# Kernel tuning notes

Hardware: AMD Instinct MI355X
Metric: run time of the kernel (lower is better)

## Reference

```python
import math
import jax, jax.numpy as jnp
import numpy as np

B_IN, B_OUT = 16, 16
F_IN, F_OUT, BATCH = 32, 64, 4
N_ALPHA, N_GAMMA = 4, 3
KERNEL_BETA = math.pi / 8.0
L_TOT = sum((2 * l + 1) ** 2 for l in range(B_OUT))  # 5456


def _lg(n):
    return math.lgamma(n + 1.0)


def _small_d(l, beta):
    """Wigner small-d matrix d^l_{m,n}(beta), [2l+1, 2l+1], Condon-Shortley phase."""
    c, s = math.cos(0.5 * beta), math.sin(0.5 * beta)
    d = np.zeros((2 * l + 1, 2 * l + 1), dtype=np.float64)
    for mi, m in enumerate(range(-l, l + 1)):
        for ni, n in enumerate(range(-l, l + 1)):
            pref = 0.5 * (_lg(l + m) + _lg(l - m) + _lg(l + n) + _lg(l - n))
            acc = 0.0
            for k in range(max(0, n - m), min(l + n, l - m) + 1):
                ln = pref - _lg(l + n - k) - _lg(k) - _lg(m - n + k) - _lg(l - m - k)
                acc += ((-1.0) ** (m - n + k)) * math.exp(ln) * (c ** (2 * l + n - m - 2 * k)) * (s ** (m - n + 2 * k))
            d[mi, ni] = acc
    return d


def _qweights(b):
    """Kostelec-Rockmore SOFT quadrature weights over the 2b beta samples."""
    k = np.arange(b)
    w = np.array([
        (2.0 / b) * math.sin(math.pi * (2 * j + 1) / (4.0 * b)) *
        np.sum(np.sin((2 * j + 1) * (2 * k + 1) * math.pi / (4.0 * b)) / (2 * k + 1))
        for j in range(2 * b)])
    return w


def _wigner_table(betas, b_out, scale_fn):
    rows = []
    for beta in betas:
        blocks = [(_small_d(l, beta) * scale_fn(l)).ravel() for l in range(b_out)]
        rows.append(np.concatenate(blocks))
    return np.stack(rows)  # [len(betas), L_TOT]


def _grid_basis(grid, b_out):
    """conj(D^l_{mn}(a,b,g)) = e^{+i m a} d^l_{mn}(b) e^{+i n g}, flattened over (l,m,n)."""
    cols = []
    for (a, bb, g) in grid:
        blocks = []
        for l in range(b_out):
            m = np.arange(-l, l + 1)
            d = _small_d(l, bb)
            ph = np.exp(1j * (m[:, None] * a + m[None, :] * g))
            blocks.append((d * ph).ravel())
        cols.append(np.concatenate(blocks))
    return np.stack(cols, axis=1)  # [L_TOT, n_grid] complex


def _freq_indices(b_out, nfft):
    ms, ns = [], []
    for l in range(b_out):
        r = np.arange(-l, l + 1)
        M, N = np.meshgrid(r, r, indexing='ij')
        ms.append(np.mod(M.ravel(), nfft))
        ns.append(np.mod(N.ravel(), nfft))
    return np.concatenate(ms), np.concatenate(ns)


def make_grid():
    alphas = [2.0 * math.pi * i / N_ALPHA for i in range(N_ALPHA)]
    gammas = [2.0 * math.pi * i / N_GAMMA for i in range(N_GAMMA)]
    return [(a, KERNEL_BETA, g) for a in alphas for g in gammas]


def setup_inputs() -> dict:
    key = jax.random.key(0)
    k1, k2 = jax.random.split(key)
    x = jax.random.normal(k1, (BATCH, F_IN, 2 * B_IN, 2 * B_IN, 2 * B_IN), jnp.float32)
    grid = make_grid()
    n_grid = len(grid)
    stdv = 1.0 / math.sqrt(n_grid * F_IN * (B_OUT ** 3) / float(B_IN ** 3))
    kernel = stdv * jax.random.normal(k2, (F_IN, F_OUT, n_grid), jnp.float32)
    bias = jnp.zeros((1, F_OUT, 1, 1, 1), jnp.float32)
    # analysis table: quadrature weight * d, with (2pi/2b)^2/(8pi^2) = 1/(8 b^2) absorbed
    betas_in = np.pi * (2 * np.arange(2 * B_IN) + 1) / (4.0 * B_IN)
    w = _qweights(B_IN) / (8.0 * B_IN ** 2)
    wig_f = _wigner_table(betas_in, B_OUT, lambda l: 1.0) * w[:, None]
    # synthesis table: (2l+1) * d, times (2b)^2 to cancel ifft2 normalization
    betas_out = np.pi * (2 * np.arange(2 * B_OUT) + 1) / (4.0 * B_OUT)
    wig_i = _wigner_table(betas_out, B_OUT, lambda l: (2 * l + 1) * (2 * B_OUT) ** 2)
    D = _grid_basis(grid, B_OUT)
    return {
        'x': x, 'kernel': kernel, 'bias': bias,
        'wigner_fwd': jnp.asarray(wig_f, jnp.float32),
        'wigner_inv': jnp.asarray(wig_i, jnp.float32),
        'D_re': jnp.asarray(D.real, jnp.float32),
        'D_im': jnp.asarray(D.imag, jnp.float32),
    }


def reference(x, kernel, bias, wigner_fwd, wigner_inv, D_re, D_im):
    batch, fin = x.shape[0], x.shape[1]
    fout = kernel.shape[1]
    midx_in, nidx_in = _freq_indices(B_OUT, 2 * B_IN)
    midx_out, nidx_out = _freq_indices(B_OUT, 2 * B_OUT)
    # --- SO3 FFT of input: FFT over (alpha, gamma), weighted beta-sum with Wigner-d ---
    Xf = jnp.fft.fft2(x.astype(jnp.complex64), axes=(-2, -1))   # [z,i,beta,ma,ng]
    Xg = Xf[..., midx_in, nidx_in]                               # [z,i,beta,L]
    xh = jnp.einsum('bl,zibl->lzi', wigner_fwd.astype(jnp.complex64), Xg)  # [L,z,i]
    # --- local FT of kernel on SO(3) grid points ---
    Dc = jax.lax.complex(D_re, D_im)                             # [L, n_grid]
    yh = jnp.einsum('lj,ioj->lio', Dc, kernel.astype(jnp.complex64))       # [L,i,o]
    # --- per-frequency block matmul (SO3_mm): z^l = x^l @ y^l, contracting f_in ---
    zs, begin = [], 0
    for l in range(B_OUT):
        n = 2 * l + 1
        xl = xh[begin:begin + n * n].reshape(n, n, batch, fin)
        yl = yh[begin:begin + n * n].reshape(n, n, fin, fout)
        zs.append(jnp.einsum('mkzi,knio->mnzo', xl, yl).reshape(n * n, batch, fout))
        begin += n * n
    zh = jnp.concatenate(zs, axis=0)                             # [L,z,o]
    # --- inverse SO3 FFT: scatter (l,m,n) -> FFT bins, ifft over (alpha,gamma) ---
    term = jnp.einsum('bl,lzo->zobl', wigner_inv.astype(jnp.complex64), zh)
    ng = 2 * B_OUT
    Zf = jnp.zeros((batch, fout, ng, ng, ng), jnp.complex64)
    Zf = Zf.at[..., midx_out, nidx_out].add(term)
    out = jnp.fft.ifft2(Zf, axes=(-2, -1)).real.astype(x.dtype)
    return out + bias
```

## Files before the change

### kernel.cpp

```cpp
#include <hip/hip_runtime.h>
#include <math.h>


typedef unsigned short u16;
typedef unsigned int   u32;
typedef __attribute__((ext_vector_type(8))) short  short8;
typedef __attribute__((ext_vector_type(4))) float  floatx4;
typedef __attribute__((ext_vector_type(2))) float  f32x2;

constexpr int LTOT = 5456;

constexpr int LB[17] = {0,1,10,35,84,165,286,455,680,969,
                        1330,1771,2300,2925,3654,4495,5456};

__device__ inline u16 f2bf(float f) {
    u32 u = __float_as_uint(f);
    u += 0x7fff + ((u >> 16) & 1);
    return (u16)(u >> 16);
}
__device__ inline u32 pack2bf(float re, float im) {
    return (u32)f2bf(re) | ((u32)f2bf(im) << 16);
}

__device__ inline short8 btr4(uint4 q, u32 sel, u32 msk) {
    uint4 t;
    t.x = __builtin_amdgcn_perm(q.x, q.x, sel) ^ msk;
    t.y = __builtin_amdgcn_perm(q.y, q.y, sel) ^ msk;
    t.z = __builtin_amdgcn_perm(q.z, q.z, sel) ^ msk;
    t.w = __builtin_amdgcn_perm(q.w, q.w, sel) ^ msk;
    return *(short8*)&t;
}

__device__ __forceinline__ f32x2 cfma(f32x2 e, f32x2 t, f32x2 acc) {
    asm("v_pk_fma_f32 %0, %1, %2, %0 op_sel:[0,0,0] op_sel_hi:[0,1,1]\n\t"
        "v_pk_fma_f32 %0, %1, %2, %0 op_sel:[1,1,0] op_sel_hi:[1,0,1] neg_lo:[0,1,0]"
        : "+v"(acc) : "v"(e), "v"(t));
    return acc;
}
__device__ __forceinline__ f32x2 cmulp(f32x2 t, f32x2 r) {
    f32x2 d;
    asm("v_pk_mul_f32 %0, %1, %2 op_sel:[0,0] op_sel_hi:[0,1]\n\t"
        "v_pk_fma_f32 %0, %1, %2, %0 op_sel:[1,1,0] op_sel_hi:[1,0,1] neg_lo:[0,1,0]"
        : "=&v"(d) : "v"(t), "v"(r));
    return d;
}
__device__ __forceinline__ f32x2 fma_bl(f32x2 w2, f32x2 v, f32x2 acc) {
    asm("v_pk_fma_f32 %0, %1, %2, %0 op_sel:[0,0,0] op_sel_hi:[0,1,1]"
        : "+v"(acc) : "v"(w2), "v"(v));
    return acc;
}
__device__ __forceinline__ f32x2 fma_bh(f32x2 w2, f32x2 v, f32x2 acc) {
    asm("v_pk_fma_f32 %0, %1, %2, %0 op_sel:[1,0,0] op_sel_hi:[1,1,1]"
        : "+v"(acc) : "v"(w2), "v"(v));
    return acc;
}

__global__ __launch_bounds__(256) void k_wtr(const float* __restrict__ w,
                                             float* __restrict__ wT) {
    int t  = blockIdx.x * 256 + threadIdx.x;
    int bq = blockIdx.y;
    if (t < LTOT) {
        float4 v;
        v.x = w[(size_t)(bq * 4 + 0) * LTOT + t];
        v.y = w[(size_t)(bq * 4 + 1) * LTOT + t];
        v.z = w[(size_t)(bq * 4 + 2) * LTOT + t];
        v.w = w[(size_t)(bq * 4 + 3) * LTOT + t];
        *(float4*)(wT + ((size_t)bq * LTOT + t) * 4) = v;
    }
}

__global__ __launch_bounds__(512) void k_fft_fwd(const float* __restrict__ x,
                                                 u32* __restrict__ Xfb) {
    __shared__ __align__(8) float xs[1088];
    __shared__ __align__(8) f32x2 Gc[1056];
    __shared__ f32x2 Wfc[32];
    int tid = threadIdx.x;
    if (tid < 32) {
        float sv, cv;
        sincosf(6.28318530717958647692f * (float)tid / 32.0f, &sv, &cv);
        f32x2 wv; wv.x = cv; wv.y = -sv;
        Wfc[tid] = wv;
    }
    const float* src = x + (size_t)blockIdx.x * 1024;
    for (int e = tid; e < 1024; e += 512) xs[(e >> 5) * 34 + (e & 31)] = src[e];
    __syncthreads();
    {
        int a = tid >> 4, k = tid & 15;
        const f32x2* rowp = (const f32x2*)&xs[a * 34];
        f32x2 r = Wfc[2 * k];
        f32x2 p0 = rowp[0];
        f32x2 E; E.x = p0.x; E.y = 0.f;
        f32x2 O; O.x = p0.y; O.y = 0.f;
        f32x2 t = r;
#pragma unroll
        for (int h = 1; h < 16; h++) {
            f32x2 p = rowp[h];
            E = fma_bl(p, t, E);
            O = fma_bh(p, t, O);
            if (h < 15) t = cmulp(t, r);
        }
        f32x2 WO = cmulp(O, Wfc[k]);
        Gc[a * 33 + k]      = E + WO;
        Gc[a * 33 + k + 16] = E - WO;
    }
    __syncthreads();
    {
        u32* dst = Xfb + (size_t)blockIdx.x * 512;
        int ng = tid & 31, ma = tid >> 5;
        f32x2 r = Wfc[2 * ma];
        f32x2 E = Gc[ng];
        f32x2 O = Gc[33 + ng];
        f32x2 t = r;
#pragma unroll
        for (int h = 1; h < 16; h++) {
            f32x2 e = Gc[(2 * h) * 33 + ng];
            f32x2 o = Gc[(2 * h + 1) * 33 + ng];
            E = cfma(e, t, E);
            O = cfma(o, t, O);
            if (h < 15) t = cmulp(t, r);
        }
        f32x2 WO = cmulp(O, Wfc[ma]);
        dst[ma * 32 + ng] = pack2bf(E.x + WO.x, E.y + WO.y);
    }
}

__global__ __launch_bounds__(256) void k_prep_B(const float* __restrict__ Dre,
                                                const float* __restrict__ Dim,
                                                const float* __restrict__ ker,
                                                u32* __restrict__ yhb) {
    __shared__ float Ds[2][24];
    int t0  = blockIdx.x * 2;
    int tid = threadIdx.x;
    if (tid < 48) {
        int rr = tid / 24, jj = tid - rr * 24;
        Ds[rr][jj] = (jj < 12) ? Dre[(t0 + rr) * 12 + jj] : Dim[(t0 + rr) * 12 + jj - 12];
    }
    __syncthreads();
    for (int rep = 0; rep < 8; rep++) {
        int io = rep * 256 + tid;
        int i  = io >> 6, o = io & 63;
        int nio = ((i >> 4) << 10) + ((o >> 5) << 9) + (((o >> 3) & 3) << 7)
                + (((i >> 2) & 3) << 5) + ((o & 7) << 2) + (i & 3);
        const float4* kp = (const float4*)(ker + io * 12);
        float4 ka = kp[0], kb = kp[1], kc = kp[2];
        float kv[12] = {ka.x, ka.y, ka.z, ka.w, kb.x, kb.y, kb.z, kb.w,
                        kc.x, kc.y, kc.z, kc.w};
#pragma unroll
        for (int rr = 0; rr < 2; rr++) {
            float sr = 0.f, si = 0.f;
#pragma unroll
            for (int j = 0; j < 12; j++) {
                sr += Ds[rr][j]      * kv[j];
                si += Ds[rr][12 + j] * kv[j];
            }
            yhb[(size_t)(t0 + rr) * 2048 + nio] = pack2bf(sr, si);
        }
    }
}

__global__ __launch_bounds__(256) void k_beta_A(const u32* __restrict__ Xfb,
                                                const float* __restrict__ wfT,
                                                u16* __restrict__ Ab) {
    int ma  = blockIdx.x >> 6;
    int zig = blockIdx.x & 63;
    int tid = threadIdx.x;
    int ng  = tid & 31;
    int lq  = (tid >> 5) & 3;
    int zil = tid >> 7;
    int zi  = zig * 2 + zil;
    int z = zi >> 5, i = zi & 31;
    int mh = (ma <= 15) ? ma : ma - 32;
    int nh = (ng <= 15) ? ng : ng - 32;
    int am = mh < 0 ? -mh : mh;
    int an = nh < 0 ? -nh : nh;
    int l0 = am > an ? am : an;
    int lb = lq * 4;

    int isconj = (ma > 16);
    int mau = isconj ? (32 - ma) : ma;
    int ngu = isconj ? ((32 - ng) & 31) : ng;
    if (mau > 15) { mau = 0; ngu = 0; }

    int tl[4];
#pragma unroll
    for (int j = 0; j < 4; j++) {
        int l = lb + j;
        tl[j] = LB[l] + (mh + l) * (2 * l + 1) + (nh + l);
    }
    float2 acc[4];
#pragma unroll
    for (int j = 0; j < 4; j++) acc[j] = make_float2(0.f, 0.f);

    const u32* xp = Xfb + (size_t)zi * 32 * 512 + mau * 32 + ngu;
    float sgn = isconj ? -1.f : 1.f;
#pragma unroll 2
    for (int bq = 0; bq < 8; bq++) {
        u32 p0 = xp[(size_t)(4 * bq + 0) * 512];
        u32 p1 = xp[(size_t)(4 * bq + 1) * 512];
        u32 p2 = xp[(size_t)(4 * bq + 2) * 512];
        u32 p3 = xp[(size_t)(4 * bq + 3) * 512];
        float vx0 = __uint_as_float(p0 << 16);
        float vy0 = sgn * __uint_as_float(p0 & 0xffff0000u);
        float vx1 = __uint_as_float(p1 << 16);
        float vy1 = sgn * __uint_as_float(p1 & 0xffff0000u);
        float vx2 = __uint_as_float(p2 << 16);
        float vy2 = sgn * __uint_as_float(p2 & 0xffff0000u);
        float vx3 = __uint_as_float(p3 << 16);
        float vy3 = sgn * __uint_as_float(p3 & 0xffff0000u);
        const float4* wq = (const float4*)(wfT + (size_t)bq * (LTOT * 4));
#pragma unroll
        for (int j = 0; j < 4; j++) {
            if (lb + j >= l0) {
                float4 w = wq[tl[j]];
                acc[j].x += w.x * vx0 + w.y * vx1 + w.z * vx2 + w.w * vx3;
                acc[j].y += w.x * vy0 + w.y * vy1 + w.z * vy2 + w.w * vy3;
            }
        }
    }
    int s_i  = i >> 4;
    int kl   = 2 * (i & 15);
    int joff = kl & 7;
    int Lhi  = (kl >> 3) << 4;
#pragma unroll
    for (int j = 0; j < 4; j++) {
        int l = lb + j;
        if (l >= l0) {
            int mi = mh + l, ni = nh + l;
            int s   = 2 * ni + s_i;
            int row = 4 * mi + z;
            u32 pack = pack2bf(acc[j].x, acc[j].y);
            size_t off = (size_t)8192 * l * l + (size_t)s * 4096
                       + ((row >> 4) << 9) + ((Lhi + (row & 15)) << 3) + joff;
            *(u32*)(Ab + off) = pack;
        }
    }
}

__global__ __launch_bounds__(256) void k_gemm(const u16* __restrict__ Ab,
                                              const u32* __restrict__ yhb,
                                              float* __restrict__ zhT) {
    __shared__ __align__(16) uint4 Bs[2][128];

    int id  = (int)blockIdx.x;
    int o5  = id & 31;
    int g5  = o5 & 7;
    int k5  = o5 >> 3;
    int flat = (id & ~31) | ((g5 & 3) + ((g5 >> 2) << 4) + (k5 << 2));
    int rem = flat, l, nl = 1;
    for (l = 15; l >= 0; l--) {
        nl = 2 * l + 1;
        int c = nl * 4;
        if (rem < c) break;
        rem -= c;
    }
    int n  = rem >> 2;
    int oq = rem & 3;
    int base = LB[l];
    const u16* Ag = Ab + (size_t)8192 * l * l;
    int G = nl;

    int tid = threadIdx.x, lane = tid & 63, w = tid >> 6;
    int cc = lane & 1;
    u32 sel = cc ? 0x01000302u : 0x03020100u;
    u32 msk = cc ? 0u          : 0x80000000u;

    const uint4* Bg = (const uint4*)yhb + (size_t)(base + n) * 512 + (oq << 6);
    const u16*   Aw = Ag + ((w << 10) | (lane << 3));
    int lu = tid & 63, lsl = tid >> 6;

    floatx4 acc[2][2];
#pragma unroll
    for (int a = 0; a < 2; a++)
#pragma unroll
        for (int b = 0; b < 2; b++) acc[a][b] = (floatx4)0.f;

#define LOADBG(gg, br) { if (tid < 128) br = Bg[(size_t)(gg) * nl * 512 + (lsl << 8) + lu]; }
#define LOADA2(gg, r0, r1, r2, r3) { \
    const u16* apx = Aw + (size_t)(gg) * 8192; \
    r0 = *(const short8*)apx;          r1 = *(const short8*)(apx + 512); \
    r2 = *(const short8*)(apx + 4096); r3 = *(const short8*)(apx + 4608); }
#define MF(a, b, c) __builtin_amdgcn_mfma_f32_16x16x32_bf16(a, b, c, 0, 0, 0)
#define GROUP(buf, A0r, A1r, A2r, A3r, gnext) { \
    __syncthreads(); \
    if (tid < 128) Bs[(buf) ^ 1][tid] = Br; \
    LOADBG(gnext, Br); \
    short8 la0 = A0r, la1 = A1r, la2 = A2r, la3 = A3r; \
    LOADA2(gnext, A0r, A1r, A2r, A3r); \
    uint4 q0 = Bs[buf][lane >> 1],       q1 = Bs[buf][32 + (lane >> 1)]; \
    uint4 q2 = Bs[buf][64 + (lane >> 1)], q3 = Bs[buf][96 + (lane >> 1)]; \
    short8 bf0 = btr4(q0, sel, msk), bf1 = btr4(q1, sel, msk); \
    short8 bf2 = btr4(q2, sel, msk), bf3 = btr4(q3, sel, msk); \
    acc[0][0] = MF(la0, bf0, acc[0][0]);  acc[1][0] = MF(la1, bf0, acc[1][0]); \
    acc[0][1] = MF(la0, bf1, acc[0][1]);  acc[1][1] = MF(la1, bf1, acc[1][1]); \
    acc[0][0] = MF(la2, bf2, acc[0][0]);  acc[1][0] = MF(la3, bf2, acc[1][0]); \
    acc[0][1] = MF(la2, bf3, acc[0][1]);  acc[1][1] = MF(la3, bf3, acc[1][1]); }

    uint4 Br;
    short8 e0, e1, e2, e3;
    short8 d0, d1, d2, d3;
    LOADBG(0, Br);
    if (tid < 128) Bs[0][tid] = Br;
    LOADBG(1, Br);
    LOADA2(0, e0, e1, e2, e3);
    LOADA2(1, d0, d1, d2, d3);

    GROUP(0, e0, e1, e2, e3, 2);
    for (int g = 1; g + 1 < G; g += 2) {
        GROUP(1, d0, d1, d2, d3, g + 2);
        GROUP(0, e0, e1, e2, e3, g + 3);
    }
#undef GROUP
#undef LOADBG
#undef LOADA2
#undef MF

    int q = lane >> 4, cn = lane & 15;
#pragma unroll
    for (int mt = 0; mt < 2; mt++) {
#pragma unroll
        for (int nt = 0; nt < 2; nt++) {
            int nu2 = (nt << 4) + cn;
            int o2  = (oq << 4) + (nu2 >> 1);
            int c2  = nu2 & 1;
#pragma unroll
            for (int r = 0; r < 4; r++) {
                int R = (w << 5) + (mt << 4) + (q << 2) + r;
                int m = R >> 2, z = R & 3;
                if (m < nl) {
                    int t  = base + m * nl + n;
                    int zo = (z << 6) + o2;
                    zhT[((size_t)zo * LTOT + t) * 2 + c2] = acc[mt][nt][r];
                }
            }
        }
    }
}

__global__ __launch_bounds__(256, 8) void k_inv2(const float2* __restrict__ zhT,
                                                 const float* __restrict__ wiT,
                                                 const float* __restrict__ bias,
                                                 float* __restrict__ out) {
    __shared__ __align__(16) f32x2 Pb[4 * 544];
    __shared__ f32x2 Wf[32];
    int tid = threadIdx.x;
    int zo = blockIdx.x & 255;
    int bq = blockIdx.x >> 8;
    int b0 = bq * 4;
    if (tid < 32) {
        float sv, cv;
        sincosf(6.28318530717958647692f * (float)tid / 32.0f, &sv, &cv);
        f32x2 wv; wv.x = cv; wv.y = sv;
        Wf[tid] = wv;
    }
    {
        int ng = tid & 31, rq = tid >> 5;
        int nh = (ng <= 15) ? ng : ng - 32;
        int an = nh < 0 ? -nh : nh;
        const f32x2* zr = (const f32x2*)zhT + (size_t)zo * LTOT;
        const f32x2* wp = (const f32x2*)wiT + (size_t)bq * (LTOT * 2);
#pragma unroll
        for (int mr = 0; mr < 2; mr++) {
            int ma = rq + 8 * mr;
            int l0 = ma > an ? ma : an;
            f32x2 a0 = (f32x2)0.f, a1 = a0, a2 = a0, a3 = a0;
#pragma unroll 4
            for (int l = 0; l < 16; l++) {
                if (l >= l0) {
                    int t = LB[l] + (ma + l) * (2 * l + 1) + (nh + l);
                    f32x2 zv = zr[t];
                    f32x2 w01 = wp[2 * t], w23 = wp[2 * t + 1];
                    a0 = fma_bl(w01, zv, a0);
                    a1 = fma_bh(w01, zv, a1);
                    a2 = fma_bl(w23, zv, a2);
                    a3 = fma_bh(w23, zv, a3);
                }
            }
            int po = ma * 34 + ng;
            Pb[po]            = a0;
            Pb[544 + po]      = a1;
            Pb[2 * 544 + po]  = a2;
            Pb[3 * 544 + po]  = a3;
        }
    }
    __syncthreads();
#pragma unroll
    for (int it = 0; it < 2; it++) {
        int task = tid + it * 256;
        int rowid = task >> 3, q = task & 7;
        f32x2* prow = &Pb[(rowid >> 4) * 544 + (rowid & 15) * 34];
        const floatx4* prow4 = (const floatx4*)prow;
        floatx4 eo0 = prow4[0];
        f32x2 Ep; Ep.x = eo0.x; Ep.y = eo0.y;
        f32x2 Op; Op.x = eo0.z; Op.y = eo0.w;
        f32x2 En = (f32x2)0.f, On = (f32x2)0.f;
        f32x2 r = Wf[2 * q];
        f32x2 t = r;
#pragma unroll
        for (int h = 1; h < 16; h++) {
            floatx4 eo = prow4[h];
            f32x2 e; e.x = eo.x; e.y = eo.y;
            f32x2 o; o.x = eo.z; o.y = eo.w;
            if (h & 1) { En = cfma(e, t, En); On = cfma(o, t, On); }
            else       { Ep = cfma(e, t, Ep); Op = cfma(o, t, Op); }
            if (h < 15) t = cmulp(t, r);
        }
        f32x2 E0 = Ep + En, E1 = Ep - En;
        f32x2 O0 = Op + On, O1 = Op - On;
        f32x2 wq = Wf[q];
        f32x2 w0 = cmulp(O0, wq);
        f32x2 u1 = cmulp(O1, wq);
        f32x2 w1; w1.x = -u1.y; w1.y = u1.x;
        prow[q]      = E0 + w0;
        prow[q + 16] = E0 - w0;
        prow[q + 8]  = E1 + w1;
        prow[q + 24] = E1 - w1;
    }
    __syncthreads();
    float bv = bias[zo & 63];
#pragma unroll
    for (int it = 0; it < 4; it++) {
        int task = tid + it * 256;
        int p = task >> 8, rr = task & 255;
        int qa = rr >> 5, g = rr & 31;
        const f32x2* pc = &Pb[p * 544];
        f32x2 r = Wf[2 * qa];
        f32x2 u = Wf[qa];
        f32x2 Uee = (f32x2)0.f, Ueo = Uee, Ve = Uee, Vo = Uee;
        f32x2 c0 = pc[g];
        {
            f32x2 c1 = pc[34 + g];
            Ve = cfma(c1, u, Ve);
        }
        f32x2 t = r;
        u = cmulp(u, r);
#pragma unroll
        for (int j = 1; j < 8; j++) {
            f32x2 ce = pc[(2 * j) * 34 + g];
            f32x2 co = pc[(2 * j + 1) * 34 + g];
            if (j & 1) { Ueo = cfma(ce, t, Ueo); Vo = cfma(co, u, Vo); }
            else       { Uee = cfma(ce, t, Uee); Ve = cfma(co, u, Ve); }
            if (j < 7) { t = cmulp(t, r); u = cmulp(u, r); }
        }
        float EaA = c0.x + 2.f * (Uee.x + Ueo.x);
        float EaB = c0.x + 2.f * (Uee.x - Ueo.x);
        float OaA = 2.f * (Ve.x + Vo.x);
        float OaB = -2.f * (Ve.y - Vo.y);
        float* dst = out + (size_t)zo * 32768 + (size_t)(b0 + p) * 1024;
        constexpr float sc = 1.f / 1024.f;
        dst[qa * 32 + g]         = (EaA + OaA) * sc + bv;
        dst[(qa + 16) * 32 + g]  = (EaA - OaA) * sc + bv;
        dst[(qa + 8) * 32 + g]   = (EaB + OaB) * sc + bv;
        dst[(qa + 24) * 32 + g]  = (EaB - OaB) * sc + bv;
    }
}

extern "C" void kernel_launch(void* const* d_in, const int* in_sizes, int n_in,
                              void* d_out, int out_size, void* d_ws, size_t ws_size,
                              hipStream_t stream) {
    const float* x    = (const float*)d_in[0];
    const float* ker  = (const float*)d_in[1];
    const float* bias = (const float*)d_in[2];
    const float* wf   = (const float*)d_in[3];
    const float* wi   = (const float*)d_in[4];
    const float* Dre  = (const float*)d_in[5];
    const float* Dim  = (const float*)d_in[6];
    float* out = (float*)d_out;

    char* ws = (char*)d_ws;
    u32*    yhb = (u32*)ws;
    u16*    Ab  = (u16*)(ws + 44695552);
    float*  zhT = (float*)(ws + 44695552 + 4194304);
    u32*    Xfb = (u32*)zhT;
    float*  wfT = (float*)(ws + 44695552 + 4194304 + 8388608);
    float*  wiT = (float*)ws;

    hipLaunchKernelGGL(k_fft_fwd, dim3(4096),  dim3(512), 0, stream, x, Xfb);
    hipLaunchKernelGGL(k_wtr,     dim3(22, 8), dim3(256), 0, stream, wf, wfT);
    hipLaunchKernelGGL(k_prep_B,  dim3(2728),  dim3(256), 0, stream, Dre, Dim, ker, yhb);
    hipLaunchKernelGGL(k_beta_A,  dim3(2048),  dim3(256), 0, stream, Xfb, wfT, Ab);
    hipLaunchKernelGGL(k_gemm,    dim3(1024),  dim3(256), 0, stream, Ab, yhb, zhT);
    hipLaunchKernelGGL(k_wtr,     dim3(22, 8), dim3(256), 0, stream, wi, wiT);
    hipLaunchKernelGGL(k_inv2,    dim3(2048),  dim3(256), 0, stream,
                       (const float2*)zhT, wiT, bias, out);
}
```

Before: 193.0 us.

## Stage X tiles in LDS and reuse Wigner weights across four channels in k_beta_A

k_beta_A now handles four (z,i) channels per 128-thread block. It first stages their forward-FFT rows for one alpha frequency into shared memory with vectorized uint4 loads. Each Wigner weight float4 is then loaded once per beta quad and applied to all four channels, which cuts repeated global weight loads and the old strided scalar loads of X. The trade-off is more accumulator registers (16 float2), an 16KB LDS tile, a barrier, and half as many blocks, each with half the threads.

Result: no change. 194.5 us (+0.8%).

```diff
diff --git a/kernel.cpp b/kernel.cpp
--- a/kernel.cpp
+++ b/kernel.cpp
@@ -158,17 +158,15 @@
     }
 }
 
-__global__ __launch_bounds__(256) void k_beta_A(const u32* __restrict__ Xfb,
+__global__ __launch_bounds__(128) void k_beta_A(const u32* __restrict__ Xfb,
                                                 const float* __restrict__ wfT,
                                                 u16* __restrict__ Ab) {
-    int ma  = blockIdx.x >> 6;
-    int zig = blockIdx.x & 63;
+    __shared__ u32 Xs[4][32][32];
+    int ma = blockIdx.x >> 5;
+    int zq = blockIdx.x & 31;
     int tid = threadIdx.x;
     int ng  = tid & 31;
-    int lq  = (tid >> 5) & 3;
-    int zil = tid >> 7;
-    int zi  = zig * 2 + zil;
-    int z = zi >> 5, i = zi & 31;
+    int lq  = tid >> 5;
     int mh = (ma <= 15) ? ma : ma - 32;
     int nh = (ng <= 15) ? ng : ng - 32;
     int am = mh < 0 ? -mh : mh;
@@ -181,57 +179,84 @@
     int ngu = isconj ? ((32 - ng) & 31) : ng;
     if (mau > 15) { mau = 0; ngu = 0; }
 
+    {
+        const u32* xsrc = Xfb + (size_t)zq * 4 * 16384 + mau * 32;
+#pragma unroll
+        for (int it = 0; it < 8; it++) {
+            int f = tid + it * 128;
+            int c = f >> 8, b = (f >> 3) & 31, g4 = (f & 7) << 2;
+            uint4 v = *(const uint4*)(xsrc + (size_t)c * 16384 + (size_t)b * 512 + g4);
+            *(uint4*)&Xs[c][b][g4] = v;
+        }
+    }
+    __syncthreads();
+
     int tl[4];
 #pragma unroll
     for (int j = 0; j < 4; j++) {
         int l = lb + j;
         tl[j] = LB[l] + (mh + l) * (2 * l + 1) + (nh + l);
     }
-    float2 acc[4];
-#pragma unroll
-    for (int j = 0; j < 4; j++) acc[j] = make_float2(0.f, 0.f);
-
-    const u32* xp = Xfb + (size_t)zi * 32 * 512 + mau * 32 + ngu;
+    float2 acc[4][4];
+#pragma unroll
+    for (int c = 0; c < 4; c++)
+#pragma unroll
+        for (int j = 0; j < 4; j++) acc[c][j] = make_float2(0.f, 0.f);
+
     float sgn = isconj ? -1.f : 1.f;
 #pragma unroll 2
     for (int bq = 0; bq < 8; bq++) {
-        u32 p0 = xp[(size_t)(4 * bq + 0) * 512];
-        u32 p1 = xp[(size_t)(4 * bq + 1) * 512];
-        u32 p2 = xp[(size_t)(4 * bq + 2) * 512];
-        u32 p3 = xp[(size_t)(4 * bq + 3) * 512];
-        float vx0 = __uint_as_float(p0 << 16);
-        float vy0 = sgn * __uint_as_float(p0 & 0xffff0000u);
-        float vx1 = __uint_as_float(p1 << 16);
-        float vy1 = sgn * __uint_as_float(p1 & 0xffff0000u);
-        float vx2 = __uint_as_float(p2 << 16);
-        float vy2 = sgn * __uint_as_float(p2 & 0xffff0000u);
-        float vx3 = __uint_as_float(p3 << 16);
-        float vy3 = sgn * __uint_as_float(p3 & 0xffff0000u);
         const float4* wq = (const float4*)(wfT + (size_t)bq * (LTOT * 4));
+        float4 w0 = make_float4(0.f, 0.f, 0.f, 0.f), w1 = w0, w2 = w0, w3 = w0;
+        if (lb + 0 >= l0) w0 = wq[tl[0]];
+        if (lb + 1 >= l0) w1 = wq[tl[1]];
+        if (lb + 2 >= l0) w2 = wq[tl[2]];
+        if (lb + 3 >= l0) w3 = wq[tl[3]];
+#pragma unroll
+        for (int c = 0; c < 4; c++) {
+            u32 p0 = Xs[c][4 * bq + 0][ngu];
+            u32 p1 = Xs[c][4 * bq + 1][ngu];
+            u32 p2 = Xs[c][4 * bq + 2][ngu];
+            u32 p3 = Xs[c][4 * bq + 3][ngu];
+            float vx0 = __uint_as_float(p0 << 16);
+            float vy0 = sgn * __uint_as_float(p0 & 0xffff0000u);
+            float vx1 = __uint_as_float(p1 << 16);
+            float vy1 = sgn * __uint_as_float(p1 & 0xffff0000u);
+            float vx2 = __uint_as_float(p2 << 16);
+            float vy2 = sgn * __uint_as_float(p2 & 0xffff0000u);
+            float vx3 = __uint_as_float(p3 << 16);
+            float vy3 = sgn * __uint_as_float(p3 & 0xffff0000u);
+            acc[c][0].x += w0.x * vx0 + w0.y * vx1 + w0.z * vx2 + w0.w * vx3;
+            acc[c][0].y += w0.x * vy0 + w0.y * vy1 + w0.z * vy2 + w0.w * vy3;
+            acc[c][1].x += w1.x * vx0 + w1.y * vx1 + w1.z * vx2 + w1.w * vx3;
+            acc[c][1].y += w1.x * vy0 + w1.y * vy1 + w1.z * vy2 + w1.w * vy3;
+            acc[c][2].x += w2.x * vx0 + w2.y * vx1 + w2.z * vx2 + w2.w * vx3;
+            acc[c][2].y += w2.x * vy0 + w2.y * vy1 + w2.z * vy2 + w2.w * vy3;
+            acc[c][3].x += w3.x * vx0 + w3.y * vx1 + w3.z * vx2 + w3.w * vx3;
+            acc[c][3].y += w3.x * vy0 + w3.y * vy1 + w3.z * vy2 + w3.w * vy3;
+        }
+    }
+
+#pragma unroll
+    for (int c = 0; c < 4; c++) {
+        int zi = zq * 4 + c;
+        int z = zi >> 5, i = zi & 31;
+        int s_i  = i >> 4;
+        int kl   = 2 * (i & 15);
+        int joff = kl & 7;
+        int Lhi  = (kl >> 3) << 4;
 #pragma unroll
         for (int j = 0; j < 4; j++) {
-            if (lb + j >= l0) {
-                float4 w = wq[tl[j]];
-                acc[j].x += w.x * vx0 + w.y * vx1 + w.z * vx2 + w.w * vx3;
-                acc[j].y += w.x * vy0 + w.y * vy1 + w.z * vy2 + w.w * vy3;
+            int l = lb + j;
+            if (l >= l0) {
+                int mi = mh + l, ni = nh + l;
+                int s   = 2 * ni + s_i;
+                int row = 4 * mi + z;
+                u32 pack = pack2bf(acc[c][j].x, acc[c][j].y);
+                size_t off = (size_t)8192 * l * l + (size_t)s * 4096
+                           + ((row >> 4) << 9) + ((Lhi + (row & 15)) << 3) + joff;
+                *(u32*)(Ab + off) = pack;
             }
-        }
-    }
-    int s_i  = i >> 4;
-    int kl   = 2 * (i & 15);
-    int joff = kl & 7;
-    int Lhi  = (kl >> 3) << 4;
-#pragma unroll
-    for (int j = 0; j < 4; j++) {
-        int l = lb + j;
-        if (l >= l0) {
-            int mi = mh + l, ni = nh + l;
-            int s   = 2 * ni + s_i;
-            int row = 4 * mi + z;
-            u32 pack = pack2bf(acc[j].x, acc[j].y);
-            size_t off = (size_t)8192 * l * l + (size_t)s * 4096
-                       + ((row >> 4) << 9) + ((Lhi + (row & 15)) << 3) + joff;
-            *(u32*)(Ab + off) = pack;
         }
     }
 }
@@ -477,7 +502,7 @@
     hipLaunchKernelGGL(k_fft_fwd, dim3(4096),  dim3(512), 0, stream, x, Xfb);
     hipLaunchKernelGGL(k_wtr,     dim3(22, 8), dim3(256), 0, stream, wf, wfT);
     hipLaunchKernelGGL(k_prep_B,  dim3(2728),  dim3(256), 0, stream, Dre, Dim, ker, yhb);
-    hipLaunchKernelGGL(k_beta_A,  dim3(2048),  dim3(256), 0, stream, Xfb, wfT, Ab);
+    hipLaunchKernelGGL(k_beta_A,  dim3(1024),  dim3(128), 0, stream, Xfb, wfT, Ab);
     hipLaunchKernelGGL(k_gemm,    dim3(1024),  dim3(256), 0, stream, Ab, yhb, zhT);
     hipLaunchKernelGGL(k_wtr,     dim3(22, 8), dim3(256), 0, stream, wi, wiT);
     hipLaunchKernelGGL(k_inv2,    dim3(2048),  dim3(256), 0, stream,
```
